# Kernel optimization log

Measured on AMD Instinct MI355X. Metric: run time of the kernel, lower is better.

The kernel has to match this reference:

```python
import jax, jax.numpy as jnp
import numpy as np

C = 256
NUM_HEADS = 8
HEAD_DIM = C // NUM_HEADS
SCALE = HEAD_DIM ** -0.5


def setup_inputs() -> dict:
    key = jax.random.key(0)
    ks = jax.random.split(key, 10)
    B, H, W = 2, 64, 64
    s = 0.02
    return {
        "spatial_feat": jax.random.normal(ks[0], (B, C, H, W), jnp.float32),
        "freq_feat": jax.random.normal(ks[1], (B, C, H, W), jnp.float32),
        "wq": jax.random.normal(ks[2], (C, C), jnp.float32) * s,
        "bq": jax.random.normal(ks[3], (C,), jnp.float32) * s,
        "wk": jax.random.normal(ks[4], (C, C), jnp.float32) * s,
        "bk": jax.random.normal(ks[5], (C,), jnp.float32) * s,
        "wv": jax.random.normal(ks[6], (C, C), jnp.float32) * s,
        "bv": jax.random.normal(ks[7], (C,), jnp.float32) * s,
        "wo": jax.random.normal(ks[8], (C, C), jnp.float32) * s,
        "bo": jax.random.normal(ks[9], (C,), jnp.float32) * s,
    }


def _proj(x, w, b):
    # 1x1 conv == channel-mixing matmul: (O,C) x (B,C,H,W) -> (B,O,H,W)
    return jnp.einsum('oc,bchw->bohw', w, x) + b[None, :, None, None]


def _heads(x, B, HW):
    return x.reshape(B, NUM_HEADS, HEAD_DIM, HW)


def _cross_attend(q_src, kv_src, wq, bq, wk, bk, wv, bv, wo, bo):
    B, Cc, H, W = q_src.shape
    HW = H * W
    q = _heads(_proj(q_src, wq, bq), B, HW)   # (B, h, d, N)
    k = _heads(_proj(kv_src, wk, bk), B, HW)
    v = _heads(_proj(kv_src, wv, bv), B, HW)
    # attn[b,h,m,n] = q[...,m] . k[...,n]
    attn = jnp.einsum('bhdm,bhdn->bhmn', q, k) * SCALE
    attn = jax.nn.softmax(attn, axis=-1)
    # out[...,m] = sum_n v[...,n] * attn[m,n]
    out = jnp.einsum('bhdn,bhmn->bhdm', v, attn)
    out = out.reshape(B, Cc, H, W)
    return _proj(out, wo, bo)


def reference(spatial_feat, freq_feat, wq, bq, wk, bk, wv, bv, wo, bo):
    spatial_attended = spatial_feat + _cross_attend(
        spatial_feat, freq_feat, wq, bq, wk, bk, wv, bv, wo, bo)
    freq_attended = freq_feat + _cross_attend(
        freq_feat, spatial_feat, wq, bq, wk, bk, wv, bv, wo, bo)
    return spatial_attended + freq_attended
```

## Files before the change

### kernel.cpp

```cpp
#include <hip/hip_runtime.h>
#include <hip/hip_bf16.h>

#define B_ 2
#define C_ 256
#define NH_ 8
#define D_ 32
#define N_ 4096
#define SCALE_ 0.17677669529663689f
#define QSC_ 0.25505277f

typedef __hip_bfloat16 bf16;
typedef __attribute__((ext_vector_type(8))) short sx8;
typedef __attribute__((ext_vector_type(4))) short sx4;
typedef __attribute__((ext_vector_type(4))) float fx4;

__device__ __forceinline__ float b2f(bf16 x) { return __bfloat162float(x); }
__device__ __forceinline__ bf16 f2b(float x) { return __float2bfloat16(x); }
__device__ __forceinline__ short fbs(float x) { bf16 h = __float2bfloat16(x); return *(short*)&h; }
__device__ __forceinline__ float sbf(short s) { bf16 h = *(bf16*)&s; return __bfloat162float(h); }
__device__ __forceinline__ void lds_fence() { asm volatile("s_waitcnt lgkmcnt(0)" ::: "memory"); }

#if __has_builtin(__builtin_amdgcn_exp2f)
__device__ __forceinline__ float fexp2(float x) { return __builtin_amdgcn_exp2f(x); }
#else
__device__ __forceinline__ float fexp2(float x) { return exp2f(x); }
#endif

__global__ __launch_bounds__(256)
void convert_x_kernel(const float* __restrict__ spatial,
                      const float* __restrict__ freq,
                      bf16* __restrict__ xb) {
  const int tid = threadIdx.x;
  const int p0 = blockIdx.x * 64;
  const int c0 = blockIdx.y * 64;
  const int z  = blockIdx.z;
  const int s = z >> 1, b = z & 1;
  const float* x = (s == 0) ? spatial : freq;

  __shared__ float ls[64][65];

  const int pp = tid & 63, cb = tid >> 6;
  #pragma unroll
  for (int i = 0; i < 16; ++i) {
    int c = cb + 4 * i;
    ls[c][pp] = x[(size_t)(b * C_ + c0 + c) * N_ + p0 + pp];
  }
  __syncthreads();

  #pragma unroll
  for (int i = 0; i < 2; ++i) {
    int j = tid + 256 * i;
    int p = j >> 3, ck = (j & 7) * 8;
    short tmp[8];
    #pragma unroll
    for (int u = 0; u < 8; ++u) tmp[u] = fbs(ls[ck + u][p]);
    *(sx8*)(xb + ((size_t)z * N_ + p0 + p) * C_ + c0 + ck) = *(sx8*)tmp;
  }
}

__global__ __launch_bounds__(256)
void convert_w_kernel(const float* __restrict__ wq, const float* __restrict__ wk,
                      const float* __restrict__ wv, const float* __restrict__ wo,
                      bf16* __restrict__ wb, bf16* __restrict__ wob) {
  int idx = blockIdx.x * 256 + threadIdx.x;
  if (idx < 196608) {
    const float* src = (idx < 65536) ? wq : (idx < 131072) ? wk : wv;
    wb[idx] = f2b(src[idx & 65535]);
  } else {
    int off = idx - 196608;
    wob[off] = f2b(wo[off]);
  }
}

__global__ __launch_bounds__(256)
void qkv_gemm_kernel(const bf16* __restrict__ wb, const bf16* __restrict__ xb,
                     const float* __restrict__ bq, const float* __restrict__ bk,
                     const float* __restrict__ bv,
                     bf16* __restrict__ qhf, bf16* __restrict__ khf,
                     bf16* __restrict__ vhf) {
  const int tid = threadIdx.x;
  const int p0 = blockIdx.x * 128;
  const int o0 = blockIdx.y * 128;
  const int z  = blockIdx.z;

  const int lane = tid & 63, w = tid >> 6;
  const int ml = lane & 15, Q4 = (lane >> 4) * 4, Q8 = (lane >> 4) * 8;
  const int ow = (w >> 1) * 64, pw = (w & 1) * 64;

  __shared__ __align__(16) short asb[128 * 72];
  __shared__ __align__(16) short bsb[128 * 72];
  __shared__ float bias_s[128];

  if (tid < 128) {
    int o = o0 + tid;
    bias_s[tid] = (o < 256) ? bq[o] : (o < 512) ? bk[o - 256] : bv[o - 512];
  }

  const fx4 z4 = {0.f, 0.f, 0.f, 0.f};
  fx4 acc[4][4];
  #pragma unroll
  for (int ot = 0; ot < 4; ++ot)
    #pragma unroll
    for (int pt = 0; pt < 4; ++pt) acc[ot][pt] = z4;

  const int sr = tid >> 1, scu = (tid & 1) * 32;
  for (int k0 = 0; k0 < 256; k0 += 64) {
    __syncthreads();
    #pragma unroll
    for (int u = 0; u < 4; ++u) {
      *(sx8*)&asb[sr * 72 + scu + u * 8] =
          *(const sx8*)&wb[(o0 + sr) * 256 + k0 + scu + u * 8];
      *(sx8*)&bsb[sr * 72 + scu + u * 8] =
          *(const sx8*)(xb + ((size_t)z * N_ + p0 + sr) * C_ + k0 + scu + u * 8);
    }
    __syncthreads();
    #pragma unroll
    for (int kk = 0; kk < 2; ++kk) {
      sx8 af[4], bfr[4];
      #pragma unroll
      for (int t = 0; t < 4; ++t)
        af[t] = *(sx8*)&asb[(ow + t * 16 + ml) * 72 + kk * 32 + Q8];
      #pragma unroll
      for (int t = 0; t < 4; ++t)
        bfr[t] = *(sx8*)&bsb[(pw + t * 16 + ml) * 72 + kk * 32 + Q8];
      #pragma unroll
      for (int ot = 0; ot < 4; ++ot)
        #pragma unroll
        for (int pt = 0; pt < 4; ++pt)
          acc[ot][pt] = __builtin_amdgcn_mfma_f32_16x16x32_bf16(
              af[ot], bfr[pt], acc[ot][pt], 0, 0, 0);
    }
  }

  if (o0 < 512) {
    bf16* dst = (o0 < 256) ? qhf : khf;
    const int ob = (o0 < 256) ? o0 : o0 - 256;
    const float scl = (o0 < 256) ? QSC_ : 1.f;
    #pragma unroll
    for (int ot = 0; ot < 4; ++ot) {
      const int og = ob + ow + ot * 16 + Q4;
      #pragma unroll
      for (int pt = 0; pt < 4; ++pt) {
        int p = p0 + pw + pt * 16 + ml;
        short tmp[4];
        #pragma unroll
        for (int r = 0; r < 4; ++r)
          tmp[r] = fbs((acc[ot][pt][r] + bias_s[ow + ot * 16 + Q4 + r]) * scl);
        *(sx4*)(dst + (((size_t)z * NH_ + (og >> 5)) * N_ + p) * D_ + (og & 31)) =
            *(sx4*)tmp;
      }
    }
  } else {
    #pragma unroll
    for (int ot = 0; ot < 4; ++ot)
      #pragma unroll
      for (int pt = 0; pt < 4; ++pt) {
        int p = p0 + pw + pt * 16 + ml;
        #pragma unroll
        for (int r = 0; r < 4; ++r) {
          int rho = (o0 - 512) + ow + ot * 16 + Q4 + r;
          int h = rho >> 5, d = rho & 31;
          size_t basev = ((size_t)z * NH_ + h) * D_ * N_;
          vhf[basev + (size_t)(((p >> 5) * 2) + (d >> 4)) * 512 +
              (d & 15) * 32 + (p & 31)] =
              f2b(acc[ot][pt][r] + bias_s[(o0 - 512) - (o0 - 512) + ow + ot * 16 + Q4 + r]);
        }
      }
  }
}

__global__ __launch_bounds__(256)
void attn_kernel(const bf16* __restrict__ qhf, const bf16* __restrict__ khf,
                 const bf16* __restrict__ vhf, bf16* __restrict__ attoT) {
  const int tid  = threadIdx.x;
  const int m0   = blockIdx.x * 128;
  const int h    = blockIdx.y;
  const int z    = blockIdx.z;
  const int s = z >> 1, b = z & 1;
  const int zo = ((1 - s) << 1) | b;

  const bf16* qz = qhf + ((size_t)z  * NH_ + h) * N_ * D_;
  const bf16* kz = khf + ((size_t)zo * NH_ + h) * N_ * D_;
  const bf16* vz = vhf + ((size_t)zo * NH_ + h) * D_ * N_;

  const int lane = tid & 63;
  const int w    = tid >> 6;
  const int ml   = lane & 15;
  const int Q4   = (lane >> 4) * 4;
  const int Q8   = (lane >> 4) * 8;

  __shared__ __align__(16) short pst[4][2][16 * 72];

  sx8 qf[2];
  #pragma unroll
  for (int s2 = 0; s2 < 2; ++s2)
    qf[s2] = *(const sx8*)(qz + (size_t)(m0 + w * 32 + s2 * 16 + ml) * D_ + Q8);

  const fx4 z4 = {0.f, 0.f, 0.f, 0.f};
  fx4 acc[2][2] = {{z4, z4}, {z4, z4}};
  float lsum[2] = {0.f, 0.f};

  for (int n0 = 0; n0 < N_; n0 += 64) {
    sx8 kf[4];
    #pragma unroll
    for (int t = 0; t < 4; ++t)
      kf[t] = *(const sx8*)(kz + (size_t)(n0 + t * 16 + ml) * D_ + Q8);
    sx8 vf[2][2];
    #pragma unroll
    for (int dt = 0; dt < 2; ++dt)
      #pragma unroll
      for (int c = 0; c < 2; ++c)
        vf[dt][c] = *(const sx8*)(vz + (size_t)(((n0 >> 5) + c) * 2 + dt) * 512 +
                                  ml * 32 + Q8);

    #pragma unroll
    for (int s2 = 0; s2 < 2; ++s2) {
      fx4 st[4];
      #pragma unroll
      for (int t = 0; t < 4; ++t)
        st[t] = __builtin_amdgcn_mfma_f32_16x16x32_bf16(kf[t], qf[s2], z4, 0, 0, 0);

      float rsum = 0.f;
      #pragma unroll
      for (int t = 0; t < 4; ++t)
        #pragma unroll
        for (int r = 0; r < 4; ++r) {
          float p = fexp2(st[t][r]);
          st[t][r] = p;
          rsum += p;
        }
      lsum[s2] += rsum;

      #pragma unroll
      for (int t = 0; t < 4; ++t) {
        sx4 pk = {fbs(st[t][0]), fbs(st[t][1]), fbs(st[t][2]), fbs(st[t][3])};
        *(sx4*)&pst[w][s2][ml * 72 + t * 16 + Q4] = pk;
      }
      lds_fence();
      sx8 pf0 = *(sx8*)&pst[w][s2][ml * 72 + 0  + Q8];
      sx8 pf1 = *(sx8*)&pst[w][s2][ml * 72 + 32 + Q8];

      #pragma unroll
      for (int dt = 0; dt < 2; ++dt) {
        fx4 a = acc[s2][dt];
        a = __builtin_amdgcn_mfma_f32_16x16x32_bf16(vf[dt][0], pf0, a, 0, 0, 0);
        a = __builtin_amdgcn_mfma_f32_16x16x32_bf16(vf[dt][1], pf1, a, 0, 0, 0);
        acc[s2][dt] = a;
      }
    }
  }

  #pragma unroll
  for (int s2 = 0; s2 < 2; ++s2) {
    float l = lsum[s2];
    l += __shfl_xor(l, 16);
    l += __shfl_xor(l, 32);
    float inv = 1.f / l;
    int col = m0 + w * 32 + s2 * 16 + ml;
    #pragma unroll
    for (int dt = 0; dt < 2; ++dt) {
      short tmp[4];
      #pragma unroll
      for (int r = 0; r < 4; ++r) tmp[r] = fbs(acc[s2][dt][r] * inv);
      *(sx4*)(attoT + ((size_t)z * N_ + col) * C_ + h * D_ + dt * 16 + Q4) =
          *(sx4*)tmp;
    }
  }
}

__global__ __launch_bounds__(256)
void out_proj_kernel(const bf16* __restrict__ wob, const bf16* __restrict__ attoT,
                     const float* __restrict__ spatial,
                     const float* __restrict__ freq,
                     const float* __restrict__ bo, float* __restrict__ out) {
  const int tid = threadIdx.x;
  const int p0 = blockIdx.x * 128;
  const int o0 = blockIdx.y * 64;
  const int b  = blockIdx.z;

  const int lane = tid & 63, w = tid >> 6;
  const int ml = lane & 15, Q4 = (lane >> 4) * 4, Q8 = (lane >> 4) * 8;
  const int ow = (w >> 1) * 32, pw = (w & 1) * 64;

  __shared__ __align__(16) short asb[64 * 72];
  __shared__ __align__(16) short bsb[128 * 72];
  __shared__ float bo_s[64];

  if (tid < 64) bo_s[tid] = 2.f * bo[o0 + tid];

  const bf16* at0 = attoT + (size_t)(0 + b) * N_ * C_;
  const bf16* at1 = attoT + (size_t)(2 + b) * N_ * C_;

  const fx4 z4 = {0.f, 0.f, 0.f, 0.f};
  fx4 acc[2][4];
  #pragma unroll
  for (int ot = 0; ot < 2; ++ot)
    #pragma unroll
    for (int pt = 0; pt < 4; ++pt) acc[ot][pt] = z4;

  for (int k0 = 0; k0 < 256; k0 += 64) {
    __syncthreads();
    #pragma unroll
    for (int i = 0; i < 2; ++i) {
      int j = tid + 256 * i;
      int r = j >> 3, cu = (j & 7) * 8;
      *(sx8*)&asb[r * 72 + cu] = *(const sx8*)&wob[(o0 + r) * 256 + k0 + cu];
    }
    #pragma unroll
    for (int i = 0; i < 4; ++i) {
      int j = tid + 256 * i;
      int p = j >> 3, cu = (j & 7) * 8;
      sx8 va = *(const sx8*)(at0 + (size_t)(p0 + p) * C_ + k0 + cu);
      sx8 vb2 = *(const sx8*)(at1 + (size_t)(p0 + p) * C_ + k0 + cu);
      short tmp[8];
      #pragma unroll
      for (int u = 0; u < 8; ++u) tmp[u] = fbs(sbf(va[u]) + sbf(vb2[u]));
      *(sx8*)&bsb[p * 72 + cu] = *(sx8*)tmp;
    }
    __syncthreads();
    #pragma unroll
    for (int kk = 0; kk < 2; ++kk) {
      sx8 af[2], bfr[4];
      #pragma unroll
      for (int t = 0; t < 2; ++t)
        af[t] = *(sx8*)&asb[(ow + t * 16 + ml) * 72 + kk * 32 + Q8];
      #pragma unroll
      for (int t = 0; t < 4; ++t)
        bfr[t] = *(sx8*)&bsb[(pw + t * 16 + ml) * 72 + kk * 32 + Q8];
      #pragma unroll
      for (int ot = 0; ot < 2; ++ot)
        #pragma unroll
        for (int pt = 0; pt < 4; ++pt)
          acc[ot][pt] = __builtin_amdgcn_mfma_f32_16x16x32_bf16(
              af[ot], bfr[pt], acc[ot][pt], 0, 0, 0);
    }
  }

  #pragma unroll
  for (int ot = 0; ot < 2; ++ot)
    #pragma unroll
    for (int pt = 0; pt < 4; ++pt) {
      int p = p0 + pw + pt * 16 + ml;
      #pragma unroll
      for (int r = 0; r < 4; ++r) {
        int ol = ow + ot * 16 + Q4 + r;
        size_t off = ((size_t)b * C_ + o0 + ol) * N_ + p;
        out[off] = acc[ot][pt][r] + bo_s[ol] + spatial[off] + freq[off];
      }
    }
}

extern "C" void kernel_launch(void* const* d_in, const int* in_sizes, int n_in,
                              void* d_out, int out_size, void* d_ws, size_t ws_size,
                              hipStream_t stream) {
  const float* spatial = (const float*)d_in[0];
  const float* freq    = (const float*)d_in[1];
  const float* wq = (const float*)d_in[2];
  const float* bq = (const float*)d_in[3];
  const float* wk = (const float*)d_in[4];
  const float* bk = (const float*)d_in[5];
  const float* wv = (const float*)d_in[6];
  const float* bv = (const float*)d_in[7];
  const float* wo = (const float*)d_in[8];
  const float* bo = (const float*)d_in[9];
  float* out = (float*)d_out;

  const size_t SZ = (size_t)2 * B_ * N_ * C_;
  bf16* xb    = (bf16*)d_ws;
  bf16* qhf   = xb + SZ;
  bf16* khf   = qhf + SZ;
  bf16* vhf   = khf + SZ;
  bf16* attoT = vhf + SZ;
  bf16* wb    = attoT + SZ;
  bf16* wob   = wb + 768 * 256;

  convert_w_kernel<<<dim3(1024), 256, 0, stream>>>(wq, wk, wv, wo, wb, wob);
  convert_x_kernel<<<dim3(N_ / 64, C_ / 64, 2 * B_), 256, 0, stream>>>(
      spatial, freq, xb);
  qkv_gemm_kernel<<<dim3(N_ / 128, 768 / 128, 2 * B_), 256, 0, stream>>>(
      wb, xb, bq, bk, bv, qhf, khf, vhf);
  attn_kernel<<<dim3(N_ / 128, NH_, 2 * B_), 256, 0, stream>>>(
      qhf, khf, vhf, attoT);
  out_proj_kernel<<<dim3(N_ / 128, C_ / 64, B_), 256, 0, stream>>>(
      wob, attoT, spatial, freq, bo, out);
}
```

Baseline: 235.2 us.

## Double-buffer K/V loads and compute softmax row sums with ones-MFMA

The attention inner loop now prefetches the next K/V tile into a second register set while computing the current one, hiding global-load latency. The per-lane exp sum and cross-lane shuffles are replaced by an MFMA against an all-ones bf16 vector, which takes the row sums from the bf16-rounded probabilities. The LDS fence is also hoisted so both s2 halves are written before a single wait. In exchange, register pressure rises and normalization uses the rounded probabilities rather than fp32 values.

```diff
diff --git a/kernel.cpp b/kernel.cpp
--- a/kernel.cpp
+++ b/kernel.cpp
@@ -158,12 +158,12 @@
         int p = p0 + pw + pt * 16 + ml;
         #pragma unroll
         for (int r = 0; r < 4; ++r) {
-          int rho = (o0 - 512) + ow + ot * 16 + Q4 + r;
+          int lo = ow + ot * 16 + Q4 + r;
+          int rho = (o0 - 512) + lo;
           int h = rho >> 5, d = rho & 31;
           size_t basev = ((size_t)z * NH_ + h) * D_ * N_;
           vhf[basev + (size_t)(((p >> 5) * 2) + (d >> 4)) * 512 +
-              (d & 15) * 32 + (p & 31)] =
-              f2b(acc[ot][pt][r] + bias_s[(o0 - 512) - (o0 - 512) + ow + ot * 16 + Q4 + r]);
+              (d & 15) * 32 + (p & 31)] = f2b(acc[ot][pt][r] + bias_s[lo]);
         }
       }
   }
@@ -196,66 +196,71 @@
   for (int s2 = 0; s2 < 2; ++s2)
     qf[s2] = *(const sx8*)(qz + (size_t)(m0 + w * 32 + s2 * 16 + ml) * D_ + Q8);
 
+  sx8 onesf;
+  #pragma unroll
+  for (int u = 0; u < 8; ++u) onesf[u] = (short)0x3F80;
+
   const fx4 z4 = {0.f, 0.f, 0.f, 0.f};
   fx4 acc[2][2] = {{z4, z4}, {z4, z4}};
-  float lsum[2] = {0.f, 0.f};
-
-  for (int n0 = 0; n0 < N_; n0 += 64) {
-    sx8 kf[4];
+  fx4 lacc[2] = {z4, z4};
+
+  sx8 kfA[4], kfB[4], vfA[2][2], vfB[2][2];
+
+  auto prefetch = [&](sx8 (&kfd)[4], sx8 (&vfd)[2][2], int nb) {
     #pragma unroll
     for (int t = 0; t < 4; ++t)
-      kf[t] = *(const sx8*)(kz + (size_t)(n0 + t * 16 + ml) * D_ + Q8);
-    sx8 vf[2][2];
+      kfd[t] = *(const sx8*)(kz + (size_t)(nb + t * 16 + ml) * D_ + Q8);
     #pragma unroll
     for (int dt = 0; dt < 2; ++dt)
       #pragma unroll
       for (int c = 0; c < 2; ++c)
-        vf[dt][c] = *(const sx8*)(vz + (size_t)(((n0 >> 5) + c) * 2 + dt) * 512 +
-                                  ml * 32 + Q8);
-
+        vfd[dt][c] = *(const sx8*)(vz + (size_t)(((nb >> 5) + c) * 2 + dt) * 512 +
+                                   ml * 32 + Q8);
+  };
+
+  auto compute = [&](const sx8 (&kfc)[4], const sx8 (&vfc)[2][2]) {
     #pragma unroll
     for (int s2 = 0; s2 < 2; ++s2) {
       fx4 st[4];
       #pragma unroll
       for (int t = 0; t < 4; ++t)
-        st[t] = __builtin_amdgcn_mfma_f32_16x16x32_bf16(kf[t], qf[s2], z4, 0, 0, 0);
-
-      float rsum = 0.f;
-      #pragma unroll
-      for (int t = 0; t < 4; ++t)
-        #pragma unroll
-        for (int r = 0; r < 4; ++r) {
-          float p = fexp2(st[t][r]);
-          st[t][r] = p;
-          rsum += p;
-        }
-      lsum[s2] += rsum;
-
+        st[t] = __builtin_amdgcn_mfma_f32_16x16x32_bf16(kfc[t], qf[s2], z4, 0, 0, 0);
       #pragma unroll
       for (int t = 0; t < 4; ++t) {
+        #pragma unroll
+        for (int r = 0; r < 4; ++r) st[t][r] = fexp2(st[t][r]);
         sx4 pk = {fbs(st[t][0]), fbs(st[t][1]), fbs(st[t][2]), fbs(st[t][3])};
         *(sx4*)&pst[w][s2][ml * 72 + t * 16 + Q4] = pk;
       }
-      lds_fence();
+    }
+    lds_fence();
+    #pragma unroll
+    for (int s2 = 0; s2 < 2; ++s2) {
       sx8 pf0 = *(sx8*)&pst[w][s2][ml * 72 + 0  + Q8];
       sx8 pf1 = *(sx8*)&pst[w][s2][ml * 72 + 32 + Q8];
-
+      lacc[s2] = __builtin_amdgcn_mfma_f32_16x16x32_bf16(onesf, pf0, lacc[s2], 0, 0, 0);
+      lacc[s2] = __builtin_amdgcn_mfma_f32_16x16x32_bf16(onesf, pf1, lacc[s2], 0, 0, 0);
       #pragma unroll
       for (int dt = 0; dt < 2; ++dt) {
         fx4 a = acc[s2][dt];
-        a = __builtin_amdgcn_mfma_f32_16x16x32_bf16(vf[dt][0], pf0, a, 0, 0, 0);
-        a = __builtin_amdgcn_mfma_f32_16x16x32_bf16(vf[dt][1], pf1, a, 0, 0, 0);
+        a = __builtin_amdgcn_mfma_f32_16x16x32_bf16(vfc[dt][0], pf0, a, 0, 0, 0);
+        a = __builtin_amdgcn_mfma_f32_16x16x32_bf16(vfc[dt][1], pf1, a, 0, 0, 0);
         acc[s2][dt] = a;
       }
     }
+  };
+
+  prefetch(kfA, vfA, 0);
+  for (int n0 = 0; n0 < N_; n0 += 128) {
+    prefetch(kfB, vfB, n0 + 64);
+    compute(kfA, vfA);
+    if (n0 + 128 < N_) prefetch(kfA, vfA, n0 + 128);
+    compute(kfB, vfB);
   }
 
   #pragma unroll
   for (int s2 = 0; s2 < 2; ++s2) {
-    float l = lsum[s2];
-    l += __shfl_xor(l, 16);
-    l += __shfl_xor(l, 32);
-    float inv = 1.f / l;
+    float inv = 1.f / lacc[s2][0];
     int col = m0 + w * 32 + s2 * 16 + ml;
     #pragma unroll
     for (int dt = 0; dt < 2; ++dt) {
```

New measurement: 237.4 us. No clear change (+0.9%).
